# Performance work log

Hardware: AMD Instinct MI355X
Metric: run time of the kernel (lower is better)

The kernel has to match this reference:

```python
import jax, jax.numpy as jnp
import numpy as np
from jax import lax

B, N = 16, 8192          # batch, points per cloud
G, K = 512, 32           # num_groups, group_size
TOKEN_DIM = 384
BN_EPS = 1e-5


def setup_inputs() -> dict:
    key = jax.random.key(0)
    ks = jax.random.split(key, 8)
    w = lambda i, shape: jax.random.normal(ks[i], shape, jnp.float32) * 0.05
    return {
        "points": jax.random.normal(ks[0], (B, N, 3), jnp.float32),
        # first_conv: Conv1d(3,128,1,bias=False) -> BN(128) -> ReLU -> Conv1d(128,256,1)
        "w1": w(1, (128, 3)),
        "bn1_gamma": jnp.ones((128,), jnp.float32),
        "bn1_beta": jnp.zeros((128,), jnp.float32),
        "bn1_mean": jnp.zeros((128,), jnp.float32),
        "bn1_var": jnp.ones((128,), jnp.float32),
        "w2": w(2, (256, 128)),
        "b2": jnp.zeros((256,), jnp.float32),
        # second_conv: Conv1d(512,512,1,bias=False) -> BN(512) -> ReLU -> Conv1d(512,384,1)
        "w3": w(3, (512, 512)),
        "bn2_gamma": jnp.ones((512,), jnp.float32),
        "bn2_beta": jnp.zeros((512,), jnp.float32),
        "bn2_mean": jnp.zeros((512,), jnp.float32),
        "bn2_var": jnp.ones((512,), jnp.float32),
        "w4": w(4, (TOKEN_DIM, 512)),
        "b4": jnp.zeros((TOKEN_DIM,), jnp.float32),
    }


def _fps(xyz, num_samples):
    """Farthest point sampling. xyz: [B,N,3] -> idx [B,num_samples] (start = point 0)."""
    b, n, _ = xyz.shape
    start = jnp.zeros((b,), jnp.int32)
    init_min = jnp.full((b, n), 1e10, xyz.dtype)

    def body(carry, _):
        min_d2, last = carry
        last_pt = jnp.take_along_axis(xyz, last[:, None, None], axis=1)  # [B,1,3]
        d2 = jnp.sum((xyz - last_pt) ** 2, axis=-1)                      # [B,N]
        min_d2 = jnp.minimum(min_d2, d2)
        nxt = jnp.argmax(min_d2, axis=-1).astype(jnp.int32)
        return (min_d2, nxt), last

    _, idx = lax.scan(body, (init_min, start), None, length=num_samples)
    return idx.T  # [B,num_samples]


def _bn(x, gamma, beta, mean, var):
    # inference batchnorm over last (channel) axis
    return (x - mean) * lax.rsqrt(var + BN_EPS) * gamma + beta


def reference(points, w1, bn1_gamma, bn1_beta, bn1_mean, bn1_var, w2, b2,
              w3, bn2_gamma, bn2_beta, bn2_mean, bn2_var, w4, b4):
    xyz = points[:, :, :3]
    fidx = _fps(xyz, G)                                       # [B,G]
    centers = jnp.take_along_axis(xyz, fidx[:, :, None], 1)   # [B,G,3]

    # brute-force KNN via squared distances [B,G,N]
    pn = jnp.sum(xyz * xyz, -1)                               # [B,N]
    cn = jnp.sum(centers * centers, -1)                       # [B,G]
    d2 = cn[:, :, None] + pn[:, None, :] - 2.0 * jnp.einsum('bgc,bnc->bgn', centers, xyz)
    _, idx = lax.top_k(-d2, K)                                # [B,G,K] nearest indices

    groups = jax.vmap(lambda p, i: p[i])(points, idx)          # [B,G,K,3]
    groups = groups - centers[:, :, None, :]                   # center-relative coords

    x = groups.reshape(B * G, K, 3)                            # [M,K,3]
    # first_conv
    f = jnp.einsum('mkc,dc->mkd', x, w1)                       # [M,K,128]
    f = jax.nn.relu(_bn(f, bn1_gamma, bn1_beta, bn1_mean, bn1_var))
    f = jnp.einsum('mkd,ed->mke', f, w2) + b2                  # [M,K,256]
    g = jnp.max(f, axis=1, keepdims=True)                      # [M,1,256]
    f = jnp.concatenate([jnp.broadcast_to(g, f.shape), f], -1) # [M,K,512]
    # second_conv
    f = jnp.einsum('mke,fe->mkf', f, w3)                       # [M,K,512]
    f = jax.nn.relu(_bn(f, bn2_gamma, bn2_beta, bn2_mean, bn2_var))
    f = jnp.einsum('mkf,of->mko', f, w4) + b4                  # [M,K,384]
    tokens = jnp.max(f, axis=1).reshape(B, G, TOKEN_DIM)
    return tokens, centers
```

## Files before the change

### kernel.cpp

```cpp
#include <hip/hip_runtime.h>
#include <stdint.h>

#define PB 16
#define PN 8192
#define PG 512
#define PK 32
#define PTOK 384
#define PM (PB*PG)
#define PMK (PM*PK)
static constexpr float BN_EPS_C = 1e-5f;

typedef short bh8  __attribute__((ext_vector_type(8)));
typedef float f32x4 __attribute__((ext_vector_type(4)));

__device__ __forceinline__ short f2bf(float f){
  unsigned u = __float_as_uint(f);
  unsigned r = u + 0x7fffu + ((u>>16)&1u);
  return (short)(r>>16);
}
__device__ __forceinline__ float bf2f(short s){
  return __uint_as_float(((unsigned)(unsigned short)s)<<16);
}
__device__ __forceinline__ void gload16(const void* g, void* l){
  __builtin_amdgcn_global_load_lds((const __attribute__((address_space(1))) unsigned int*)g,
                                   (__attribute__((address_space(3))) unsigned int*)l,
                                   16, 0, 0);
}

__global__ __launch_bounds__(1024, 4) void fps_kernel(const float* __restrict__ points,
                                                      float* __restrict__ centers){
#pragma clang fp contract(off)
  const int b = blockIdx.x;
  const int t = threadIdx.x;
  const float* P = points + (size_t)b*PN*3;
  __shared__ float4 Lc[PN];
  __shared__ unsigned short sidx[PN];
  __shared__ int shist[512];
  __shared__ int spart[64];
  __shared__ unsigned long long swa[3];
  if (t < 512) shist[t] = 0;
  if (t < 3)   swa[t] = 0ull;
  __syncthreads();
  int mycell[8];
#pragma unroll
  for (int i=0;i<8;i++){
    int j = i*1024 + t;
    float x=P[j*3+0], y=P[j*3+1], z=P[j*3+2];
    Lc[j] = make_float4(x,y,z,0.f);
    int qx=(int)fminf(fmaxf((x+4.f)*1.0f,0.f),7.f);
    int qy=(int)fminf(fmaxf((y+4.f)*1.0f,0.f),7.f);
    int qz=(int)fminf(fmaxf((z+4.f)*1.0f,0.f),7.f);
    int mc = (qx&1)|((qx&2)<<2)|((qx&4)<<4)
           | ((qy&1)<<1)|((qy&2)<<3)|((qy&4)<<5)
           | ((qz&1)<<2)|((qz&2)<<4)|((qz&4)<<6);
    mycell[i]=mc;
    atomicAdd(&shist[mc],1);
  }
  __syncthreads();
  if (t < 64){
    int acc=0;
#pragma unroll
    for (int k=0;k<8;k++){ int h=shist[t*8+k]; shist[t*8+k]=acc; acc+=h; }
    spart[t]=acc;
  }
  __syncthreads();
  if (t==0){ int acc=0; for (int k=0;k<64;k++){ int h=spart[k]; spart[k]=acc; acc+=h; } }
  __syncthreads();
  if (t < 64){
    int off=spart[t];
#pragma unroll
    for (int k=0;k<8;k++) shist[t*8+k] += off;
  }
  __syncthreads();
#pragma unroll
  for (int i=0;i<8;i++){
    int j = i*1024 + t;
    int r = atomicAdd(&shist[mycell[i]],1);
    sidx[r] = (unsigned short)j;
  }
  __syncthreads();
  float px[8],py[8],pz[8],md[8]; int lowc[8];
  float tlx=1e30f,tly=1e30f,tlz=1e30f,thx=-1e30f,thy=-1e30f,thz=-1e30f;
#pragma unroll
  for (int i=0;i<8;i++){
    int oj = sidx[t*8+i];
    float4 p4 = Lc[oj];
    float x=p4.x, y=p4.y, z=p4.z;
    px[i]=x; py[i]=y; pz[i]=z; md[i]=1e10f; lowc[i]=PN-1-oj;
    tlx=fminf(tlx,x); thx=fmaxf(thx,x);
    tly=fminf(tly,y); thy=fmaxf(thy,y);
    tlz=fminf(tlz,z); thz=fmaxf(thz,z);
  }
#pragma unroll
  for (int off=32; off; off>>=1){
    tlx=fminf(tlx,__shfl_xor(tlx,off)); thx=fmaxf(thx,__shfl_xor(thx,off));
    tly=fminf(tly,__shfl_xor(tly,off)); thy=fmaxf(thy,__shfl_xor(thy,off));
    tlz=fminf(tlz,__shfl_xor(tlz,off)); thz=fmaxf(thz,__shfl_xor(thz,off));
  }
  unsigned long long wkey = ((unsigned long long)0x7F800000u)<<32;
  float cx=P[0], cy=P[1], cz=P[2];
  if (t==0){ float* c = centers + (size_t)b*PG*3; c[0]=cx; c[1]=cy; c[2]=cz; }
  const int lane = t & 63;
  __syncthreads();
  for (int g=1; g<PG; g++){
    const int sl = g%3, ns = (g+1)%3;
    float ddx=fmaxf(fmaxf(tlx-cx, cx-thx),0.f);
    float ddy=fmaxf(fmaxf(tly-cy, cy-thy),0.f);
    float ddz=fmaxf(fmaxf(tlz-cz, cz-thz),0.f);
    float dmin2=((ddx*ddx+ddy*ddy)+ddz*ddz)*0.999999f;
    if (!(dmin2 >= __uint_as_float((unsigned)(wkey>>32)))){
      unsigned long long bk = 0ull;
#pragma unroll
      for (int i=0;i<8;i++){
        float dx=px[i]-cx, dy=py[i]-cy, dz=pz[i]-cz;
        float d2 = (dx*dx + dy*dy) + dz*dz;
        md[i] = fminf(md[i], d2);
        unsigned long long ki = ((unsigned long long)__float_as_uint(md[i])<<32)
                              | (unsigned)lowc[i];
        if (ki > bk) bk = ki;
      }
#pragma unroll
      for (int mask=32; mask; mask>>=1){
        unsigned long long o = __shfl_xor(bk, mask);
        if (o > bk) bk = o;
      }
      wkey = bk;
    }
    if (lane==0) atomicMax(&swa[sl], wkey);
    if (t==0) swa[ns] = 0ull;
    __syncthreads();
    unsigned long long w = swa[sl];
    int j = PN-1 - (int)(w & 0xFFFFFFFFu);
    float4 c4 = Lc[j];
    cx = c4.x; cy = c4.y; cz = c4.z;
    if (t==0){ float* cc = centers + ((size_t)b*PG + g)*3; cc[0]=cx; cc[1]=cy; cc[2]=cz; }
  }
}

__global__ __launch_bounds__(256) void knn_kernel(const float* __restrict__ points,
                                                  const float* __restrict__ centers,
                                                  float* __restrict__ groups){
#pragma clang fp contract(off)
  const int m = blockIdx.x;
  const int b = m >> 9;
  const int t = threadIdx.x;
  const float* P = points + (size_t)b*PN*3;
  const float* c = centers + (size_t)m*3;
  const float cx=c[0], cy=c[1], cz=c[2];
  const float cn = (cx*cx + cy*cy) + cz*cz;
  unsigned long long key[PK];
#pragma unroll
  for (int i=0;i<PK;i++){
    int j = i*256 + t;
    float x=P[j*3+0], y=P[j*3+1], z=P[j*3+2];
    float pn = (x*x + y*y) + z*z;
    float e  = (cx*x + cy*y) + cz*z;
    float d2 = (cn + pn) - 2.0f*e;
    unsigned u = __float_as_uint(d2);
    u ^= (u & 0x80000000u) ? 0xFFFFFFFFu : 0x80000000u;
    key[i] = ((unsigned long long)u << 32) | (unsigned)j;
  }
  unsigned long long lmin = key[0];
#pragma unroll
  for (int i=1;i<PK;i++) if (key[i] < lmin) lmin = key[i];
  __shared__ unsigned long long swk[2][4];
  __shared__ int s_idx[PK];
  const int lane = t & 63, wid = t >> 6;
  for (int it=0; it<PK; it++){
    unsigned long long v = lmin;
#pragma unroll
    for (int off=32; off; off>>=1){
      unsigned long long o = __shfl_down(v, off);
      if (o < v) v = o;
    }
    if (lane==0) swk[it&1][wid] = v;
    __syncthreads();
    unsigned long long w = swk[it&1][0];
#pragma unroll
    for (int q=1;q<4;q++) if (swk[it&1][q] < w) w = swk[it&1][q];
    int wj = (int)(w & 0xFFFFFFFFull);
    if (t==0) s_idx[it] = wj;
    if ((wj & 255) == t){
#pragma unroll
      for (int i=0;i<PK;i++) if (key[i] == w) key[i] = ~0ull;
      lmin = key[0];
#pragma unroll
      for (int i=1;i<PK;i++) if (key[i] < lmin) lmin = key[i];
    }
  }
  __syncthreads();
  if (t < PK*3){
    int k = t/3, cc = t - k*3;
    int j = s_idx[k];
    groups[((size_t)m*PK + k)*3 + cc] = P[j*3+cc] - c[cc];
  }
}

__global__ __launch_bounds__(512, 2) void mlp_kernel(const float* __restrict__ grp,
                                                     const float* __restrict__ w1,
                                                     const float* __restrict__ sc1,
                                                     const float* __restrict__ sh1,
                                                     const short* __restrict__ w2b,
                                                     const float* __restrict__ b2,
                                                     const short* __restrict__ w3ab,
                                                     const short* __restrict__ w3bb,
                                                     const float* __restrict__ sc2,
                                                     const float* __restrict__ sh2,
                                                     const short* __restrict__ w4b,
                                                     const float* __restrict__ b4,
                                                     float* __restrict__ tokens){
  __shared__ __align__(16) short s_f1f3[16384];
  __shared__ __align__(16) short s_f2[32768];
  __shared__ __align__(16) short s_g[1024];
  __shared__ __align__(16) short s_bst[24576];
  const int t = threadIdx.x;
  const int lane = t & 63, wid = t >> 6;
  const int mh = wid >> 1, nq = wid & 1;
  const int B0 = blockIdx.x * 128;
  const int G0 = blockIdx.x * 4;
  const int srow = lane >> 2;
  const int scol = (lane & 3) * 8;
  const int frow = lane & 15;
  const int fk   = (lane >> 4) * 8;
  const int rb   = (lane >> 4) * 4;
  const int cb   = lane & 15;

  {
    int r = t & 127, dg = t >> 7;
    float x0 = grp[(size_t)(B0+r)*3 + 0];
    float x1 = grp[(size_t)(B0+r)*3 + 1];
    float x2 = grp[(size_t)(B0+r)*3 + 2];
#pragma unroll
    for (int dd=0; dd<32; dd++){
      int d = dg*32 + dd;
      float a = x0*w1[d*3+0] + x1*w1[d*3+1] + x2*w1[d*3+2];
      float y = a*sc1[d] + sh1[d];
      s_f1f3[dg*4096 + r*32 + dd] = f2bf(fmaxf(y, 0.f));
    }
  }
  __syncthreads();

  {
    f32x4 accB[2][8] = {};
    for (int k0=0; k0<128; k0+=64){
      for (int cc=wid; cc<32; cc+=8){
        int sub = cc & 1, rc = cc >> 1;
        int r = rc*16 + srow;
        gload16(w2b + (size_t)r*128 + k0 + sub*32 + scol, &s_bst[sub*8192 + rc*512]);
      }
      __syncthreads();
#pragma unroll
      for (int sub=0; sub<2; sub++){
        int kc = (k0 + sub*32) >> 5;
        bh8 af[2], bf[8];
#pragma unroll
        for (int i=0;i<2;i++)
          af[i] = *(const bh8*)&s_f1f3[kc*4096 + (mh*32 + i*16 + frow)*32 + fk];
#pragma unroll
        for (int j=0;j<8;j++)
          bf[j] = *(const bh8*)&s_bst[sub*8192 + (nq*128 + j*16 + frow)*32 + fk];
#pragma unroll
        for (int i=0;i<2;i++)
#pragma unroll
          for (int j=0;j<8;j++)
            accB[i][j] = __builtin_amdgcn_mfma_f32_16x16x32_bf16(af[i], bf[j], accB[i][j], 0,0,0);
      }
      __syncthreads();
    }
#pragma unroll
    for (int i=0;i<2;i++)
#pragma unroll
      for (int j=0;j<8;j++){
        int col = nq*128 + j*16 + cb;
#pragma unroll
        for (int r=0;r<4;r++){
          int row = mh*32 + i*16 + rb + r;
          s_f2[(col>>5)*4096 + row*32 + (col&31)] = f2bf(accB[i][j][r] + b2[col]);
        }
      }
  }
  __syncthreads();

  {
#pragma unroll
    for (int task=0; task<2; task++){
      int g = (t>>8) + task*2;
      int col = t & 255;
      int kc = col >> 5, c5 = col & 31;
      float mx = -3.4e38f;
#pragma unroll
      for (int kk=0; kk<PK; kk++)
        mx = fmaxf(mx, bf2f(s_f2[kc*4096 + (g*32 + kk)*32 + c5]));
      s_g[g*256 + col] = f2bf(mx);
    }
  }
  __syncthreads();

  f32x4 acc4[2][12] = {};
  for (int nc=0; nc<4; nc++){
    f32x4 acc3[2][4] = {};
    for (int k0=0; k0<512; k0+=64){
      const short* w3s = (k0 < 256) ? w3ab : w3bb;
      int kk0 = (k0 < 256) ? k0 : (k0 - 256);
      for (int cc=wid; cc<16; cc+=8){
        int sub = cc & 1, rc = cc >> 1;
        int r = nc*128 + rc*16 + srow;
        gload16(w3s + (size_t)r*256 + kk0 + sub*32 + scol, &s_bst[sub*4096 + rc*512]);
      }
      __syncthreads();
#pragma unroll
      for (int sub=0; sub<2; sub++){
        int k = k0 + sub*32;
        bh8 af[2], bf[4];
        if (k < 256){
#pragma unroll
          for (int i=0;i<2;i++)
            af[i] = *(const bh8*)&s_g[mh*256 + k + fk];
        } else {
          int kc = (k - 256) >> 5;
#pragma unroll
          for (int i=0;i<2;i++)
            af[i] = *(const bh8*)&s_f2[kc*4096 + (mh*32 + i*16 + frow)*32 + fk];
        }
#pragma unroll
        for (int j=0;j<4;j++)
          bf[j] = *(const bh8*)&s_bst[sub*4096 + (nq*64 + j*16 + frow)*32 + fk];
#pragma unroll
        for (int i=0;i<2;i++)
#pragma unroll
          for (int j=0;j<4;j++)
            acc3[i][j] = __builtin_amdgcn_mfma_f32_16x16x32_bf16(af[i], bf[j], acc3[i][j], 0,0,0);
      }
      __syncthreads();
    }
#pragma unroll
    for (int i=0;i<2;i++)
#pragma unroll
      for (int j=0;j<4;j++){
        int cl = nq*64 + j*16 + cb;
        int f  = nc*128 + cl;
        float s = sc2[f], h = sh2[f];
#pragma unroll
        for (int r=0;r<4;r++){
          int row = mh*32 + i*16 + rb + r;
          float v = acc3[i][j][r]*s + h;
          s_f1f3[(cl>>5)*4096 + row*32 + (cl&31)] = f2bf(fmaxf(v, 0.f));
        }
      }
    __syncthreads();
    for (int kk0=0; kk0<128; kk0+=64){
      for (int cc=wid; cc<48; cc+=8){
        int sub = cc & 1, rc = cc >> 1;
        int r = rc*16 + srow;
        gload16(w4b + (size_t)r*512 + nc*128 + kk0 + sub*32 + scol, &s_bst[sub*12288 + rc*512]);
      }
      __syncthreads();
#pragma unroll
      for (int sub=0; sub<2; sub++){
        int kc = (kk0 + sub*32) >> 5;
        bh8 af[2], bf[12];
#pragma unroll
        for (int i=0;i<2;i++)
          af[i] = *(const bh8*)&s_f1f3[kc*4096 + (mh*32 + i*16 + frow)*32 + fk];
#pragma unroll
        for (int j=0;j<12;j++)
          bf[j] = *(const bh8*)&s_bst[sub*12288 + (nq*192 + j*16 + frow)*32 + fk];
#pragma unroll
        for (int i=0;i<2;i++)
#pragma unroll
          for (int j=0;j<12;j++)
            acc4[i][j] = __builtin_amdgcn_mfma_f32_16x16x32_bf16(af[i], bf[j], acc4[i][j], 0,0,0);
      }
      __syncthreads();
    }
  }

#pragma unroll
  for (int j=0;j<12;j++){
    int col = nq*192 + j*16 + cb;
    float mx = -3.4e38f;
#pragma unroll
    for (int i=0;i<2;i++)
#pragma unroll
      for (int r=0;r<4;r++)
        mx = fmaxf(mx, acc4[i][j][r]);
    mx = fmaxf(mx, __shfl_xor(mx, 16));
    mx = fmaxf(mx, __shfl_xor(mx, 32));
    if (lane < 16)
      tokens[(size_t)(G0 + mh)*PTOK + col] = mx + b4[col];
  }
}

__global__ __launch_bounds__(256) void prep_kernel(const float* __restrict__ w2,
    const float* __restrict__ w3, const float* __restrict__ w4,
    const float* __restrict__ g1, const float* __restrict__ be1,
    const float* __restrict__ mu1, const float* __restrict__ va1,
    const float* __restrict__ g2, const float* __restrict__ be2,
    const float* __restrict__ mu2, const float* __restrict__ va2,
    short* __restrict__ w2b, short* __restrict__ w3ab, short* __restrict__ w3bb,
    short* __restrict__ w4b, float* __restrict__ sc1, float* __restrict__ sh1,
    float* __restrict__ sc2, float* __restrict__ sh2){
  int i = blockIdx.x*256 + threadIdx.x;
  if (i < 256*128) w2b[i] = f2bf(w2[i]);
  if (i < 512*512){
    int f = i >> 9, e = i & 511;
    short v = f2bf(w3[i]);
    if (e < 256) w3ab[f*256 + e] = v; else w3bb[f*256 + (e-256)] = v;
  }
  if (i < 384*512) w4b[i] = f2bf(w4[i]);
  if (i < 128){ float s = g1[i]*rsqrtf(va1[i] + BN_EPS_C); sc1[i]=s; sh1[i]=be1[i]-mu1[i]*s; }
  if (i < 512){ float s = g2[i]*rsqrtf(va2[i] + BN_EPS_C); sc2[i]=s; sh2[i]=be2[i]-mu2[i]*s; }
}

extern "C" void kernel_launch(void* const* d_in, const int* in_sizes, int n_in,
                              void* d_out, int out_size, void* d_ws, size_t ws_size,
                              hipStream_t stream){
  const float* points = (const float*)d_in[0];
  const float* w1  = (const float*)d_in[1];
  const float* g1  = (const float*)d_in[2];
  const float* be1 = (const float*)d_in[3];
  const float* mu1 = (const float*)d_in[4];
  const float* va1 = (const float*)d_in[5];
  const float* w2  = (const float*)d_in[6];
  const float* b2  = (const float*)d_in[7];
  const float* w3  = (const float*)d_in[8];
  const float* g2  = (const float*)d_in[9];
  const float* be2 = (const float*)d_in[10];
  const float* mu2 = (const float*)d_in[11];
  const float* va2 = (const float*)d_in[12];
  const float* w4  = (const float*)d_in[13];
  const float* b4  = (const float*)d_in[14];
  float* tokens  = (float*)d_out;
  float* centers = (float*)d_out + (size_t)PM*PTOK;

  char* ws = (char*)d_ws;
  float* grp  = (float*)(ws + 0);
  short* w2b  = (short*)(ws + 3145728ull);
  short* w3ab = (short*)(ws + 3211264ull);
  short* w3bb = (short*)(ws + 3473408ull);
  short* w4b  = (short*)(ws + 3735552ull);
  float* sc1  = (float*)(ws + 4128768ull);
  float* sh1  = (float*)(ws + 4129280ull);
  float* sc2  = (float*)(ws + 4129792ull);
  float* sh2  = (float*)(ws + 4131840ull);

  prep_kernel<<<1024, 256, 0, stream>>>(w2, w3, w4, g1, be1, mu1, va1, g2, be2, mu2, va2,
                                        w2b, w3ab, w3bb, w4b, sc1, sh1, sc2, sh2);
  fps_kernel<<<PB, 1024, 0, stream>>>(points, centers);
  knn_kernel<<<PM, 256, 0, stream>>>(points, centers, grp);
  mlp_kernel<<<PMK/128, 512, 0, stream>>>(grp, w1, sc1, sh1, w2b, b2,
                                          w3ab, w3bb, sc2, sh2, w4b, b4, tokens);
}
```

Baseline: 1.220 ms.

## Fuse FPS and KNN into persistent kernel with progress-flag pipelining

Merges the farthest-point-sampling and KNN kernels into one persistent launch. The first 16 blocks run FPS and publish progress every 4 centers through a release-store flag, while 240 worker blocks pull tasks from an atomic queue and spin until the centers they need are ready. KNN grouping therefore overlaps with the long serial FPS loop instead of waiting for it to finish. The KNN keys are also shrunk to 32 bits with the index kept separately, and four centers are handled per 1024-thread block. The cost is a dependence on co-residency of the FPS blocks with the spinning workers, plus atomic polling overhead and a large static LDS footprint in every block.

```diff
diff --git a/kernel.cpp b/kernel.cpp
--- a/kernel.cpp
+++ b/kernel.cpp
@@ -8,6 +8,8 @@
 #define PTOK 384
 #define PM (PB*PG)
 #define PMK (PM*PK)
+#define NWORK 240
+#define NTASK (PM/4)
 static constexpr float BN_EPS_C = 1e-5f;
 
 typedef short bh8  __attribute__((ext_vector_type(8)));
@@ -27,172 +29,210 @@
                                    16, 0, 0);
 }
 
-__global__ __launch_bounds__(1024, 4) void fps_kernel(const float* __restrict__ points,
-                                                      float* __restrict__ centers){
+__global__ __launch_bounds__(1024, 4) void mega2_kernel(
+    const float* __restrict__ points, float* __restrict__ centers,
+    int* __restrict__ prog, int* __restrict__ qhead,
+    float* __restrict__ grp){
 #pragma clang fp contract(off)
-  const int b = blockIdx.x;
+  __shared__ __align__(16) char SMEM[150528];
   const int t = threadIdx.x;
-  const float* P = points + (size_t)b*PN*3;
-  __shared__ float4 Lc[PN];
-  __shared__ unsigned short sidx[PN];
-  __shared__ int shist[512];
-  __shared__ int spart[64];
-  __shared__ unsigned long long swa[3];
-  if (t < 512) shist[t] = 0;
-  if (t < 3)   swa[t] = 0ull;
-  __syncthreads();
-  int mycell[8];
-#pragma unroll
-  for (int i=0;i<8;i++){
-    int j = i*1024 + t;
-    float x=P[j*3+0], y=P[j*3+1], z=P[j*3+2];
-    Lc[j] = make_float4(x,y,z,0.f);
-    int qx=(int)fminf(fmaxf((x+4.f)*1.0f,0.f),7.f);
-    int qy=(int)fminf(fmaxf((y+4.f)*1.0f,0.f),7.f);
-    int qz=(int)fminf(fmaxf((z+4.f)*1.0f,0.f),7.f);
-    int mc = (qx&1)|((qx&2)<<2)|((qx&4)<<4)
-           | ((qy&1)<<1)|((qy&2)<<3)|((qy&4)<<5)
-           | ((qz&1)<<2)|((qz&2)<<4)|((qz&4)<<6);
-    mycell[i]=mc;
-    atomicAdd(&shist[mc],1);
-  }
-  __syncthreads();
-  if (t < 64){
-    int acc=0;
-#pragma unroll
-    for (int k=0;k<8;k++){ int h=shist[t*8+k]; shist[t*8+k]=acc; acc+=h; }
-    spart[t]=acc;
-  }
-  __syncthreads();
-  if (t==0){ int acc=0; for (int k=0;k<64;k++){ int h=spart[k]; spart[k]=acc; acc+=h; } }
-  __syncthreads();
-  if (t < 64){
-    int off=spart[t];
-#pragma unroll
-    for (int k=0;k<8;k++) shist[t*8+k] += off;
-  }
-  __syncthreads();
-#pragma unroll
-  for (int i=0;i<8;i++){
-    int j = i*1024 + t;
-    int r = atomicAdd(&shist[mycell[i]],1);
-    sidx[r] = (unsigned short)j;
-  }
-  __syncthreads();
-  float px[8],py[8],pz[8],md[8]; int lowc[8];
-  float tlx=1e30f,tly=1e30f,tlz=1e30f,thx=-1e30f,thy=-1e30f,thz=-1e30f;
-#pragma unroll
-  for (int i=0;i<8;i++){
-    int oj = sidx[t*8+i];
-    float4 p4 = Lc[oj];
-    float x=p4.x, y=p4.y, z=p4.z;
-    px[i]=x; py[i]=y; pz[i]=z; md[i]=1e10f; lowc[i]=PN-1-oj;
-    tlx=fminf(tlx,x); thx=fmaxf(thx,x);
-    tly=fminf(tly,y); thy=fmaxf(thy,y);
-    tlz=fminf(tlz,z); thz=fmaxf(thz,z);
-  }
-#pragma unroll
-  for (int off=32; off; off>>=1){
-    tlx=fminf(tlx,__shfl_xor(tlx,off)); thx=fmaxf(thx,__shfl_xor(thx,off));
-    tly=fminf(tly,__shfl_xor(tly,off)); thy=fmaxf(thy,__shfl_xor(thy,off));
-    tlz=fminf(tlz,__shfl_xor(tlz,off)); thz=fmaxf(thz,__shfl_xor(thz,off));
-  }
-  unsigned long long wkey = ((unsigned long long)0x7F800000u)<<32;
-  float cx=P[0], cy=P[1], cz=P[2];
-  if (t==0){ float* c = centers + (size_t)b*PG*3; c[0]=cx; c[1]=cy; c[2]=cz; }
   const int lane = t & 63;
-  __syncthreads();
-  for (int g=1; g<PG; g++){
-    const int sl = g%3, ns = (g+1)%3;
-    float ddx=fmaxf(fmaxf(tlx-cx, cx-thx),0.f);
-    float ddy=fmaxf(fmaxf(tly-cy, cy-thy),0.f);
-    float ddz=fmaxf(fmaxf(tlz-cz, cz-thz),0.f);
-    float dmin2=((ddx*ddx+ddy*ddy)+ddz*ddz)*0.999999f;
-    if (!(dmin2 >= __uint_as_float((unsigned)(wkey>>32)))){
-      unsigned long long bk = 0ull;
-#pragma unroll
-      for (int i=0;i<8;i++){
-        float dx=px[i]-cx, dy=py[i]-cy, dz=pz[i]-cz;
-        float d2 = (dx*dx + dy*dy) + dz*dz;
-        md[i] = fminf(md[i], d2);
-        unsigned long long ki = ((unsigned long long)__float_as_uint(md[i])<<32)
-                              | (unsigned)lowc[i];
-        if (ki > bk) bk = ki;
-      }
-#pragma unroll
-      for (int mask=32; mask; mask>>=1){
-        unsigned long long o = __shfl_xor(bk, mask);
-        if (o > bk) bk = o;
-      }
-      wkey = bk;
-    }
-    if (lane==0) atomicMax(&swa[sl], wkey);
-    if (t==0) swa[ns] = 0ull;
-    __syncthreads();
-    unsigned long long w = swa[sl];
-    int j = PN-1 - (int)(w & 0xFFFFFFFFu);
-    float4 c4 = Lc[j];
-    cx = c4.x; cy = c4.y; cz = c4.z;
-    if (t==0){ float* cc = centers + ((size_t)b*PG + g)*3; cc[0]=cx; cc[1]=cy; cc[2]=cz; }
-  }
-}
-
-__global__ __launch_bounds__(256) void knn_kernel(const float* __restrict__ points,
-                                                  const float* __restrict__ centers,
-                                                  float* __restrict__ groups){
-#pragma clang fp contract(off)
-  const int m = blockIdx.x;
-  const int b = m >> 9;
-  const int t = threadIdx.x;
-  const float* P = points + (size_t)b*PN*3;
-  const float* c = centers + (size_t)m*3;
-  const float cx=c[0], cy=c[1], cz=c[2];
-  const float cn = (cx*cx + cy*cy) + cz*cz;
-  unsigned long long key[PK];
-#pragma unroll
-  for (int i=0;i<PK;i++){
-    int j = i*256 + t;
-    float x=P[j*3+0], y=P[j*3+1], z=P[j*3+2];
-    float pn = (x*x + y*y) + z*z;
-    float e  = (cx*x + cy*y) + cz*z;
-    float d2 = (cn + pn) - 2.0f*e;
-    unsigned u = __float_as_uint(d2);
-    u ^= (u & 0x80000000u) ? 0xFFFFFFFFu : 0x80000000u;
-    key[i] = ((unsigned long long)u << 32) | (unsigned)j;
-  }
-  unsigned long long lmin = key[0];
-#pragma unroll
-  for (int i=1;i<PK;i++) if (key[i] < lmin) lmin = key[i];
-  __shared__ unsigned long long swk[2][4];
-  __shared__ int s_idx[PK];
-  const int lane = t & 63, wid = t >> 6;
-  for (int it=0; it<PK; it++){
-    unsigned long long v = lmin;
+
+  if (blockIdx.x < PB){
+    const int b = blockIdx.x;
+    const float* P = points + (size_t)b*PN*3;
+    float4* Lc = (float4*)SMEM;
+    unsigned short* sidx = (unsigned short*)(SMEM + 131072);
+    int* shist = (int*)(SMEM + 147456);
+    int* spart = (int*)(SMEM + 149504);
+    unsigned long long* swa = (unsigned long long*)(SMEM + 149760);
+    if (t < 512) shist[t] = 0;
+    if (t < 3)   swa[t] = 0ull;
+    __syncthreads();
+    int mycell[8];
+#pragma unroll
+    for (int i=0;i<8;i++){
+      int j = i*1024 + t;
+      float x=P[j*3+0], y=P[j*3+1], z=P[j*3+2];
+      Lc[j] = make_float4(x,y,z,0.f);
+      int qx=(int)fminf(fmaxf((x+4.f)*1.0f,0.f),7.f);
+      int qy=(int)fminf(fmaxf((y+4.f)*1.0f,0.f),7.f);
+      int qz=(int)fminf(fmaxf((z+4.f)*1.0f,0.f),7.f);
+      int mc = (qx&1)|((qx&2)<<2)|((qx&4)<<4)
+             | ((qy&1)<<1)|((qy&2)<<3)|((qy&4)<<5)
+             | ((qz&1)<<2)|((qz&2)<<4)|((qz&4)<<6);
+      mycell[i]=mc;
+      atomicAdd(&shist[mc],1);
+    }
+    __syncthreads();
+    if (t < 64){
+      int acc=0;
+#pragma unroll
+      for (int k=0;k<8;k++){ int h=shist[t*8+k]; shist[t*8+k]=acc; acc+=h; }
+      spart[t]=acc;
+    }
+    __syncthreads();
+    if (t==0){ int acc=0; for (int k=0;k<64;k++){ int h=spart[k]; spart[k]=acc; acc+=h; } }
+    __syncthreads();
+    if (t < 64){
+      int off=spart[t];
+#pragma unroll
+      for (int k=0;k<8;k++) shist[t*8+k] += off;
+    }
+    __syncthreads();
+#pragma unroll
+    for (int i=0;i<8;i++){
+      int j = i*1024 + t;
+      int r = atomicAdd(&shist[mycell[i]],1);
+      sidx[r] = (unsigned short)j;
+    }
+    __syncthreads();
+    float px[8],py[8],pz[8],md[8]; int lowc[8];
+    float tlx=1e30f,tly=1e30f,tlz=1e30f,thx=-1e30f,thy=-1e30f,thz=-1e30f;
+#pragma unroll
+    for (int i=0;i<8;i++){
+      int oj = sidx[t*8+i];
+      float4 p4 = Lc[oj];
+      float x=p4.x, y=p4.y, z=p4.z;
+      px[i]=x; py[i]=y; pz[i]=z; md[i]=1e10f; lowc[i]=PN-1-oj;
+      tlx=fminf(tlx,x); thx=fmaxf(thx,x);
+      tly=fminf(tly,y); thy=fmaxf(thy,y);
+      tlz=fminf(tlz,z); thz=fmaxf(thz,z);
+    }
 #pragma unroll
     for (int off=32; off; off>>=1){
-      unsigned long long o = __shfl_down(v, off);
-      if (o < v) v = o;
-    }
-    if (lane==0) swk[it&1][wid] = v;
-    __syncthreads();
-    unsigned long long w = swk[it&1][0];
-#pragma unroll
-    for (int q=1;q<4;q++) if (swk[it&1][q] < w) w = swk[it&1][q];
-    int wj = (int)(w & 0xFFFFFFFFull);
-    if (t==0) s_idx[it] = wj;
-    if ((wj & 255) == t){
-#pragma unroll
-      for (int i=0;i<PK;i++) if (key[i] == w) key[i] = ~0ull;
-      lmin = key[0];
-#pragma unroll
-      for (int i=1;i<PK;i++) if (key[i] < lmin) lmin = key[i];
-    }
-  }
-  __syncthreads();
-  if (t < PK*3){
-    int k = t/3, cc = t - k*3;
-    int j = s_idx[k];
-    groups[((size_t)m*PK + k)*3 + cc] = P[j*3+cc] - c[cc];
+      tlx=fminf(tlx,__shfl_xor(tlx,off)); thx=fmaxf(thx,__shfl_xor(thx,off));
+      tly=fminf(tly,__shfl_xor(tly,off)); thy=fmaxf(thy,__shfl_xor(thy,off));
+      tlz=fminf(tlz,__shfl_xor(tlz,off)); thz=fmaxf(thz,__shfl_xor(thz,off));
+    }
+    unsigned long long wkey = ((unsigned long long)0x7F800000u)<<32;
+    float cx=P[0], cy=P[1], cz=P[2];
+    if (t==0){ float* c = centers + (size_t)b*PG*3; c[0]=cx; c[1]=cy; c[2]=cz; }
+    __syncthreads();
+    for (int g=1; g<PG; g++){
+      const int sl = g%3, ns = (g+1)%3;
+      float ddx=fmaxf(fmaxf(tlx-cx, cx-thx),0.f);
+      float ddy=fmaxf(fmaxf(tly-cy, cy-thy),0.f);
+      float ddz=fmaxf(fmaxf(tlz-cz, cz-thz),0.f);
+      float dmin2=((ddx*ddx+ddy*ddy)+ddz*ddz)*0.999999f;
+      if (!(dmin2 >= __uint_as_float((unsigned)(wkey>>32)))){
+        unsigned long long bk = 0ull;
+#pragma unroll
+        for (int i=0;i<8;i++){
+          float dx=px[i]-cx, dy=py[i]-cy, dz=pz[i]-cz;
+          float d2 = (dx*dx + dy*dy) + dz*dz;
+          md[i] = fminf(md[i], d2);
+          unsigned long long ki = ((unsigned long long)__float_as_uint(md[i])<<32)
+                                | (unsigned)lowc[i];
+          if (ki > bk) bk = ki;
+        }
+#pragma unroll
+        for (int mask=32; mask; mask>>=1){
+          unsigned long long o = __shfl_xor(bk, mask);
+          if (o > bk) bk = o;
+        }
+        wkey = bk;
+      }
+      if (lane==0) atomicMax(&swa[sl], wkey);
+      if (t==0) swa[ns] = 0ull;
+      __syncthreads();
+      unsigned long long w = swa[sl];
+      int j = PN-1 - (int)(w & 0xFFFFFFFFu);
+      float4 c4 = Lc[j];
+      cx = c4.x; cy = c4.y; cz = c4.z;
+      if (t==0){
+        float* cc = centers + ((size_t)b*PG + g)*3;
+        cc[0]=cx; cc[1]=cy; cc[2]=cz;
+        if ((g & 3) == 3)
+          __hip_atomic_store(prog + b, g + 1, __ATOMIC_RELEASE, __HIP_MEMORY_SCOPE_AGENT);
+      }
+    }
+  }
+
+  unsigned long long* ks_k = (unsigned long long*)(SMEM + 149504);
+  int*   ks_idx = (int*)(SMEM + 149760);
+  float* ks_c   = (float*)(SMEM + 150272);
+  int*   s_task = (int*)(SMEM + 150320);
+
+  for(;;){
+    if (t == 0){
+      int id = atomicAdd(qhead, 1);
+      s_task[0] = id;
+      if (id < NTASK){
+        int bb = id & (PB-1), qq = id >> 4;
+        int need = qq*4 + 4;
+        while (__hip_atomic_load(prog + bb, __ATOMIC_ACQUIRE, __HIP_MEMORY_SCOPE_AGENT) < need)
+          __builtin_amdgcn_s_sleep(10);
+      }
+    }
+    __syncthreads();
+    const int id = s_task[0];
+    if (id >= NTASK) break;
+    const int b = id & (PB-1), q = id >> 4;
+    const int m0 = b*PG + q*4;
+    const float* P = points + (size_t)b*PN*3;
+    const int sub = t >> 8, tt = t & 255;
+
+    if (tt == 0){
+      const float* cp = centers + (size_t)(m0 + sub)*3;
+      ks_c[sub*3+0] = __hip_atomic_load(cp+0, __ATOMIC_ACQUIRE, __HIP_MEMORY_SCOPE_AGENT);
+      ks_c[sub*3+1] = __hip_atomic_load(cp+1, __ATOMIC_ACQUIRE, __HIP_MEMORY_SCOPE_AGENT);
+      ks_c[sub*3+2] = __hip_atomic_load(cp+2, __ATOMIC_ACQUIRE, __HIP_MEMORY_SCOPE_AGENT);
+    }
+    __syncthreads();
+    {
+      const float cx=ks_c[sub*3+0], cy=ks_c[sub*3+1], cz=ks_c[sub*3+2];
+      const float cn = (cx*cx + cy*cy) + cz*cz;
+      unsigned key[PK];
+#pragma unroll
+      for (int i=0;i<PK;i++){
+        int j = i*256 + tt;
+        float x=P[j*3+0], y=P[j*3+1], z=P[j*3+2];
+        float pn = (x*x + y*y) + z*z;
+        float e  = (cx*x + cy*y) + cz*z;
+        float d2 = (cn + pn) - 2.0f*e;
+        unsigned u = __float_as_uint(d2);
+        u ^= (u & 0x80000000u) ? 0xFFFFFFFFu : 0x80000000u;
+        key[i] = u;
+      }
+      unsigned lmin = key[0]; int li = 0;
+#pragma unroll
+      for (int i=1;i<PK;i++) if (key[i] < lmin){ lmin = key[i]; li = i; }
+      unsigned long long lkey = ((unsigned long long)lmin << 32)
+                              | (unsigned)(li*256 + tt);
+      const int widx = tt >> 6;
+      for (int it=0; it<PK; it++){
+        unsigned long long v = lkey;
+#pragma unroll
+        for (int off=32; off; off>>=1){
+          unsigned long long o = __shfl_down(v, off);
+          if (o < v) v = o;
+        }
+        if (lane==0) ks_k[sub*8 + (it&1)*4 + widx] = v;
+        __syncthreads();
+        unsigned long long w = ks_k[sub*8 + (it&1)*4 + 0];
+#pragma unroll
+        for (int qq=1;qq<4;qq++){
+          unsigned long long o = ks_k[sub*8 + (it&1)*4 + qq];
+          if (o < w) w = o;
+        }
+        int wj = (int)(w & 0xFFFFFFFFull);
+        if (tt==0) ks_idx[sub*32 + it] = wj;
+        if ((wj & 255) == tt){
+          key[wj >> 8] = 0xFFFFFFFFu;
+          lmin = key[0]; li = 0;
+#pragma unroll
+          for (int i=1;i<PK;i++) if (key[i] < lmin){ lmin = key[i]; li = i; }
+          lkey = ((unsigned long long)lmin << 32) | (unsigned)(li*256 + tt);
+        }
+      }
+      __syncthreads();
+      if (tt < PK*3){
+        int k = tt/3, c = tt - k*3;
+        int j = ks_idx[sub*32 + k];
+        grp[((size_t)(m0 + sub)*PK + k)*3 + c] = P[j*3+c] - ks_c[sub*3+c];
+      }
+    }
   }
 }
 
@@ -399,7 +439,8 @@
     const float* __restrict__ mu2, const float* __restrict__ va2,
     short* __restrict__ w2b, short* __restrict__ w3ab, short* __restrict__ w3bb,
     short* __restrict__ w4b, float* __restrict__ sc1, float* __restrict__ sh1,
-    float* __restrict__ sc2, float* __restrict__ sh2){
+    float* __restrict__ sc2, float* __restrict__ sh2,
+    int* __restrict__ prog, int* __restrict__ qhead){
   int i = blockIdx.x*256 + threadIdx.x;
   if (i < 256*128) w2b[i] = f2bf(w2[i]);
   if (i < 512*512){
@@ -410,6 +451,8 @@
   if (i < 384*512) w4b[i] = f2bf(w4[i]);
   if (i < 128){ float s = g1[i]*rsqrtf(va1[i] + BN_EPS_C); sc1[i]=s; sh1[i]=be1[i]-mu1[i]*s; }
   if (i < 512){ float s = g2[i]*rsqrtf(va2[i] + BN_EPS_C); sc2[i]=s; sh2[i]=be2[i]-mu2[i]*s; }
+  if (i < PB) prog[i] = 0;
+  if (i == PB) qhead[0] = 0;
 }
 
 extern "C" void kernel_launch(void* const* d_in, const int* in_sizes, int n_in,
@@ -443,11 +486,13 @@
   float* sh1  = (float*)(ws + 4129280ull);
   float* sc2  = (float*)(ws + 4129792ull);
   float* sh2  = (float*)(ws + 4131840ull);
+  int*   prog = (int*)(ws + 4133888ull);
+  int*   qhead= (int*)(ws + 4133952ull);
 
   prep_kernel<<<1024, 256, 0, stream>>>(w2, w3, w4, g1, be1, mu1, va1, g2, be2, mu2, va2,
-                                        w2b, w3ab, w3bb, w4b, sc1, sh1, sc2, sh2);
-  fps_kernel<<<PB, 1024, 0, stream>>>(points, centers);
-  knn_kernel<<<PM, 256, 0, stream>>>(points, centers, grp);
+                                        w2b, w3ab, w3bb, w4b, sc1, sh1, sc2, sh2,
+                                        prog, qhead);
+  mega2_kernel<<<PB + NWORK, 1024, 0, stream>>>(points, centers, prog, qhead, grp);
   mlp_kernel<<<PMK/128, 512, 0, stream>>>(grp, w1, sc1, sh1, w2b, b2,
                                           w3ab, w3bb, sc2, sh2, w4b, b4, tokens);
 }
```

Result: faster. 1.049 ms (-14.0%).
